# Kernel optimization log

Measured on AMD Instinct MI355X. Metric: run time of the kernel, lower is better.

The kernel has to match this reference:

```python
import jax, jax.numpy as jnp
import numpy as np
from jax import lax

MAX_W = 4           # max_subword_block_width
DOWNSAMPLE = 2      # downsample_rate


def setup_inputs() -> dict:
    key = jax.random.key(0)
    k1, k2, k3, k4 = jax.random.split(key, 4)
    B, E, L, K = 8, 512, 4096, 5
    x = jax.random.normal(k1, (B, E, L), dtype=jnp.float32)
    conv_w = jax.random.normal(k2, (E, E, K), dtype=jnp.float32) * (1.0 / np.sqrt(E * K))
    conv_b = jax.random.normal(k3, (E,), dtype=jnp.float32) * 0.02
    score_w = jax.random.normal(k4, (E,), dtype=jnp.float32) * (1.0 / np.sqrt(E))
    return {"x": x, "conv_w": conv_w, "conv_b": conv_b, "score_w": score_w}


def reference(x, conv_w, conv_b, score_w):
    B, E, L = x.shape  # `length` captured BEFORE conv, as in the torch code
    # pre-GBST conv, VALID padding: length becomes L - K + 1
    y = lax.conv_general_dilated(
        x, conv_w, window_strides=(1,), padding='VALID',
        dimension_numbers=('NCH', 'OIH', 'NCH')) + conv_b[None, :, None]
    L2 = y.shape[-1]
    seqs, scores = [], []
    for w in range(1, MAX_W + 1):
        pad = (-L2) % w
        yp = jnp.pad(y, ((0, 0), (0, 0), (0, pad)))  # zero-pad to multiple of w
        nb = yp.shape[-1] // w
        pooled = yp.reshape(B, E, nb, w).mean(-1)          # avg_pool1d(kernel=w, stride=w)
        sc = jnp.einsum('ben,e->bn', pooled, score_w)      # Linear(E,1,bias=False)
        rs = jnp.repeat(pooled, w, axis=-1)                # repeat_interleave
        rsc = jnp.repeat(sc, w, axis=-1)
        cur = rs.shape[-1]
        if cur < L:  # re-pad with zeros up to the ORIGINAL (pre-conv) length
            rs = jnp.pad(rs, ((0, 0), (0, 0), (0, L - cur)))
            rsc = jnp.pad(rsc, ((0, 0), (0, L - cur)))
        seqs.append(rs[:, :, :L])
        scores.append(rsc[:, :L])
    S = jnp.stack(seqs, axis=-1)                           # [B,E,L,W]
    A = jax.nn.softmax(jnp.stack(scores, axis=-1), axis=-1)  # [B,L,W]
    out = jnp.einsum('belw,blw->bel', S, A)                # softmax-weighted combine
    r = DOWNSAMPLE
    Ld = (L // r) * r
    out = out[:, :, :Ld].reshape(B, E, L // r, r).mean(-1)  # final avg_pool1d
    return out
```

## Files before the change

### kernel.cpp

```cpp
#include <hip/hip_runtime.h>
#include <stdint.h>

#define E_DIM 512
#define L_IN  4096
#define L_OUT 4092
#define KW    5
#define B_DIM 8
#define L2P   4096
#define L_DS  2048
#define LP    4160

typedef __attribute__((ext_vector_type(8))) short short8;
typedef __attribute__((ext_vector_type(4))) float f32x4;

__device__ __forceinline__ unsigned short f2bf(float f) {
    uint32_t u = __float_as_uint(f);
    u += 0x7fffu + ((u >> 16) & 1);
    return (unsigned short)(u >> 16);
}
__device__ __forceinline__ float bf2f(unsigned short h) {
    return __uint_as_float((uint32_t)h << 16);
}

__global__ __launch_bounds__(256)
void xt_kernel(const float* __restrict__ x, unsigned short* __restrict__ Xt)
{
    const int b  = blockIdx.z;
    const int i0 = blockIdx.y * 64;
    const int l0 = blockIdx.x * 64;
    __shared__ float T[64][65];
    const int tid = threadIdx.x;

    const int ir = tid >> 4;
    const int cq = (tid & 15) * 4;
    #pragma unroll
    for (int jj = 0; jj < 4; ++jj) {
        int i = jj * 16 + ir;
        float4 v = make_float4(0.f, 0.f, 0.f, 0.f);
        if (l0 < L_IN)
            v = *reinterpret_cast<const float4*>(
                &x[((size_t)b * E_DIM + i0 + i) * L_IN + l0 + cq]);
        T[i][cq + 0] = v.x; T[i][cq + 1] = v.y;
        T[i][cq + 2] = v.z; T[i][cq + 3] = v.w;
    }
    __syncthreads();
    const int h  = tid & 31;
    const int rq = tid >> 5;
    #pragma unroll
    for (int j = 0; j < 8; ++j) {
        int lr = j * 8 + rq;
        ushort2 o;
        o.x = f2bf(T[2 * h][lr]);
        o.y = f2bf(T[2 * h + 1][lr]);
        *reinterpret_cast<ushort2*>(
            &Xt[((size_t)b * LP + l0 + lr) * E_DIM + i0 + 2 * h]) = o;
    }
}

__global__ __launch_bounds__(256)
void wt_kernel(const float* __restrict__ w, unsigned short* __restrict__ Wt)
{
    int idx = blockIdx.x * 256 + threadIdx.x;
    if (idx >= E_DIM * E_DIM) return;
    #pragma unroll
    for (int k = 0; k < KW; ++k)
        Wt[(size_t)k * E_DIM * E_DIM + idx] = f2bf(w[(size_t)idx * KW + k]);
}

#define XB_BYTES 17408
#define N_XCH    (XB_BYTES / 1024)
#define WOFF     (2 * XB_BYTES)
#define WS_BYTES (5 * 128 * 64)
#define N_WCH    (WS_BYTES / 1024)
#define LDS_BYTES (WOFF + WS_BYTES)

__global__ __launch_bounds__(256, 2)
void conv_mfma(const unsigned short* __restrict__ Xt,
               const unsigned short* __restrict__ Wt,
               const float* __restrict__ bias,
               const float* __restrict__ sw,
               unsigned short* __restrict__ y,
               float* __restrict__ sp)
{
    __shared__ __align__(16) unsigned char lds[LDS_BYTES];
    const int l0 = blockIdx.x * 256;
    const int e0 = blockIdx.y * 128;
    const int b  = blockIdx.z;
    const int tid  = threadIdx.x;
    const int lane = tid & 63;
    const int wv   = tid >> 6;
    const int wr = wv >> 1, wc = wv & 1;
    const int lr = lane & 15, lg = lane >> 4;
    const int ln4r = lane >> 2;
    const int xswz = ((lane & 3) ^ ((lane >> 3) & 3)) * 8;

    const int aBase = WOFF + (wr * 64 + lr) * 64
                    + ((lg ^ ((lr >> 1) & 3)) << 4);
    int bBase[KW];
    #pragma unroll
    for (int kt = 0; kt < KW; ++kt)
        bBase[kt] = (wc * 128 + lr + kt) * 64
                  + ((lg ^ (((lr + kt) >> 1) & 3)) << 4);

    const unsigned short* xt_base =
        Xt + ((size_t)b * LP + l0) * E_DIM + xswz;

    auto stageX = [&](int buf, int i0) {
        for (int cch = wv; cch < N_XCH; cch += 4) {
            int row = cch * 16 + ln4r;
            const unsigned short* gp = xt_base + (size_t)row * E_DIM + i0;
            __builtin_amdgcn_global_load_lds(
                (const __attribute__((address_space(1))) void*)gp,
                (__attribute__((address_space(3))) void*)(lds + buf * XB_BYTES + cch * 1024),
                16, 0, 0);
        }
    };
    auto stageW = [&](int i0) {
        for (int cch = wv; cch < N_WCH; cch += 4) {
            int rk = cch * 16 + ln4r;
            int k = rk >> 7, er = rk & 127;
            const unsigned short* gp =
                Wt + ((size_t)k * E_DIM + e0 + er) * E_DIM + i0 + xswz;
            __builtin_amdgcn_global_load_lds(
                (const __attribute__((address_space(1))) void*)gp,
                (__attribute__((address_space(3))) void*)(lds + WOFF + cch * 1024),
                16, 0, 0);
        }
    };

    f32x4 acc[4][8] = {};

    stageX(0, 0);
    stageW(0);
    asm volatile("s_waitcnt vmcnt(0)" ::: "memory");
    __builtin_amdgcn_s_barrier();

    for (int ks = 0; ks < 16; ++ks) {
        const int par = ks & 1;
        if (ks < 15) stageX(par ^ 1, (ks + 1) * 32);

        #pragma unroll
        for (int kt = 0; kt < KW; ++kt) {
            short8 aF[4], bF[8];
            #pragma unroll
            for (int m = 0; m < 4; ++m)
                aF[m] = *reinterpret_cast<const short8*>(
                    &lds[aBase + (kt * 128 + m * 16) * 64]);
            #pragma unroll
            for (int n = 0; n < 8; ++n)
                bF[n] = *reinterpret_cast<const short8*>(
                    &lds[par * XB_BYTES + bBase[kt] + n * 1024]);
            #pragma unroll
            for (int m = 0; m < 4; ++m)
                #pragma unroll
                for (int n = 0; n < 8; ++n)
                    acc[m][n] = __builtin_amdgcn_mfma_f32_16x16x32_bf16(
                        aF[m], bF[n], acc[m][n], 0, 0, 0);
        }

        if (ks < 15) {
            __builtin_amdgcn_s_barrier();
            stageW((ks + 1) * 32);
            asm volatile("s_waitcnt vmcnt(0)" ::: "memory");
            __builtin_amdgcn_s_barrier();
        }
    }

    float spn[8] = {};
    #pragma unroll
    for (int m = 0; m < 4; ++m)
        #pragma unroll
        for (int q = 0; q < 4; ++q) {
            int e = e0 + wr * 64 + m * 16 + lg * 4 + q;
            float bv = bias[e];
            float wv_s = sw[e];
            unsigned short* yr =
                y + ((size_t)b * E_DIM + e) * L2P + l0 + wc * 128 + lr;
            #pragma unroll
            for (int n = 0; n < 8; ++n) {
                float v = acc[m][n][q] + bv;
                yr[n * 16] = f2bf(v);
                spn[n] = fmaf(v, wv_s, spn[n]);
            }
        }
    #pragma unroll
    for (int n = 0; n < 8; ++n) {
        float p = spn[n];
        p += __shfl_xor(p, 16);
        p += __shfl_xor(p, 32);
        if (lane < 16) {
            int l = l0 + wc * 128 + n * 16 + lane;
            sp[((size_t)b * L2P + l) * 8 + blockIdx.y * 2 + wr] = p;
        }
    }
}

__global__ __launch_bounds__(256)
void weight_kernel(const float* __restrict__ sp, float* __restrict__ A)
{
    const int b  = blockIdx.y;
    const int l0 = blockIdx.x * 256;
    const int tid = threadIdx.x;
    __shared__ float sl[260];

    for (int idx = tid; idx < 260; idx += 256) {
        int l = l0 - 2 + idx;
        float v = 0.f;
        if (l >= 0 && l < L_OUT) {
            const float* p = &sp[((size_t)b * L2P + l) * 8];
            v = ((p[0] + p[1]) + (p[2] + p[3])) + ((p[4] + p[5]) + (p[6] + p[7]));
        }
        sl[idx] = v;
    }
    __syncthreads();

    const int l = l0 + tid;
    if (l >= L_OUT) return;
    #define SL(i) sl[(i) - (l0 - 2)]
    float sc0 = SL(l);
    int n2 = l & ~1;
    float sc1 = 0.5f * (SL(n2) + SL(n2 + 1));
    int n3 = (l / 3) * 3;
    float sc2 = (1.f / 3.f) * (SL(n3) + SL(n3 + 1) + SL(n3 + 2));
    int n4 = l & ~3;
    float sc3 = 0.25f * (SL(n4) + SL(n4 + 1) + SL(n4 + 2) + SL(n4 + 3));
    #undef SL

    float m  = fmaxf(fmaxf(sc0, sc1), fmaxf(sc2, sc3));
    float e0 = __expf(sc0 - m), e1 = __expf(sc1 - m);
    float e2 = __expf(sc2 - m), e3 = __expf(sc3 - m);
    float inv = 1.f / (e0 + e1 + e2 + e3);

    float4 av = make_float4(e0 * inv, e1 * inv, e2 * inv, e3 * inv);
    *reinterpret_cast<float4*>(&A[((size_t)b * L2P + l) * 4]) = av;
}

typedef __attribute__((ext_vector_type(8))) unsigned short u16x8;

__global__ __launch_bounds__(256)
void combine_kernel(const unsigned short* __restrict__ y,
                    const float* __restrict__ A, float* __restrict__ out)
{
    const int e = blockIdx.x;
    const int b = blockIdx.y;
    const int tid = threadIdx.x;
    __shared__ float ys[L2P];

    const unsigned short* yrow = y + ((size_t)b * E_DIM + e) * L2P;
    #pragma unroll
    for (int j = 0; j < 2; ++j) {
        int base = (tid + j * 256) * 8;
        u16x8 v = *reinterpret_cast<const u16x8*>(&yrow[base]);
        #pragma unroll
        for (int t = 0; t < 8; ++t) ys[base + t] = bf2f(v[t]);
    }
    __syncthreads();

    const float* Ab = A + (size_t)b * L2P * 4;
    float* orow = out + ((size_t)b * E_DIM + e) * L_DS;
    #pragma unroll
    for (int j = 0; j < 8; ++j) {
        int m = tid + j * 256;
        float acc = 0.f;
        #pragma unroll
        for (int r = 0; r < 2; ++r) {
            int l = 2 * m + r;
            if (l < L_OUT) {
                const float4 a4 = *reinterpret_cast<const float4*>(&Ab[l * 4]);
                float t = a4.x * ys[l];
                int n2 = l & ~1;
                t += a4.y * 0.5f * (ys[n2] + ys[n2 + 1]);
                int n3 = (l / 3) * 3;
                t += a4.z * (1.f / 3.f) * (ys[n3] + ys[n3 + 1] + ys[n3 + 2]);
                int n4 = l & ~3;
                t += a4.w * 0.25f * (ys[n4] + ys[n4 + 1] + ys[n4 + 2] + ys[n4 + 3]);
                acc += t;
            }
        }
        orow[m] = 0.5f * acc;
    }
}

extern "C" void kernel_launch(void* const* d_in, const int* in_sizes, int n_in,
                              void* d_out, int out_size, void* d_ws, size_t ws_size,
                              hipStream_t stream)
{
    const float* x  = (const float*)d_in[0];
    const float* w  = (const float*)d_in[1];
    const float* bb = (const float*)d_in[2];
    const float* sw = (const float*)d_in[3];
    float* out = (float*)d_out;

    unsigned short* Y = (unsigned short*)d_ws;
    float* SP = (float*)(Y + (size_t)B_DIM * E_DIM * L2P);
    float* A  = SP + (size_t)B_DIM * L2P * 8;
    unsigned short* Xt = (unsigned short*)(A + (size_t)B_DIM * L2P * 4);
    unsigned short* Wt = Xt + (size_t)B_DIM * LP * E_DIM;

    xt_kernel<<<dim3(LP / 64, E_DIM / 64, B_DIM), 256, 0, stream>>>(x, Xt);
    wt_kernel<<<dim3(E_DIM * E_DIM / 256), 256, 0, stream>>>(w, Wt);
    conv_mfma<<<dim3(L2P / 256, E_DIM / 128, B_DIM), 256, 0, stream>>>(Xt, Wt, bb, sw, Y, SP);
    weight_kernel<<<dim3(L2P / 256, B_DIM), 256, 0, stream>>>(SP, A);
    combine_kernel<<<dim3(E_DIM, B_DIM), 256, 0, stream>>>(Y, A, out);
}
```

Measured before the change: 119.7 us.

## Pipeline weight taps through a three-slot LDS ring with per-tap barriers

The full 5-tap weight slab, which used to be loaded with an exposed vmcnt(0) wait after each K-step, is replaced by a 3-slot ring of per-tap weight slices. Each slice is prefetched two taps ahead and overlaps with the MFMA work, using partial vmcnt waits. This shrinks LDS use, which may allow more residency, and hides the weight-load latency. In exchange there are two barriers per tap instead of per K-step, plus s_setprio around the MFMA bursts.

Measured after the change: 116.1 us. 3.0% less time.

```diff
diff --git a/kernel.cpp b/kernel.cpp
--- a/kernel.cpp
+++ b/kernel.cpp
@@ -21,6 +21,11 @@
 __device__ __forceinline__ float bf2f(unsigned short h) {
     return __uint_as_float((uint32_t)h << 16);
 }
+__device__ __forceinline__ int mod3(int v) {
+    if (v >= 6) v -= 6;
+    if (v >= 3) v -= 3;
+    return v;
+}
 
 __global__ __launch_bounds__(256)
 void xt_kernel(const float* __restrict__ x, unsigned short* __restrict__ Xt)
@@ -67,12 +72,10 @@
         Wt[(size_t)k * E_DIM * E_DIM + idx] = f2bf(w[(size_t)idx * KW + k]);
 }
 
-#define XB_BYTES 17408
-#define N_XCH    (XB_BYTES / 1024)
-#define WOFF     (2 * XB_BYTES)
-#define WS_BYTES (5 * 128 * 64)
-#define N_WCH    (WS_BYTES / 1024)
-#define LDS_BYTES (WOFF + WS_BYTES)
+#define XB_BYTES  17408
+#define WOFF      (2 * XB_BYTES)
+#define WSL_BYTES 8192
+#define LDS_BYTES (WOFF + 3 * WSL_BYTES)
 
 __global__ __launch_bounds__(256, 2)
 void conv_mfma(const unsigned short* __restrict__ Xt,
@@ -94,8 +97,7 @@
     const int ln4r = lane >> 2;
     const int xswz = ((lane & 3) ^ ((lane >> 3) & 3)) * 8;
 
-    const int aBase = WOFF + (wr * 64 + lr) * 64
-                    + ((lg ^ ((lr >> 1) & 3)) << 4);
+    const int aOff = (wr * 64 + lr) * 64 + ((lg ^ ((lr >> 1) & 3)) << 4);
     int bBase[KW];
     #pragma unroll
     for (int kt = 0; kt < KW; ++kt)
@@ -106,7 +108,7 @@
         Xt + ((size_t)b * LP + l0) * E_DIM + xswz;
 
     auto stageX = [&](int buf, int i0) {
-        for (int cch = wv; cch < N_XCH; cch += 4) {
+        for (int cch = wv; cch < 17; cch += 4) {
             int row = cch * 16 + ln4r;
             const unsigned short* gp = xt_base + (size_t)row * E_DIM + i0;
             __builtin_amdgcn_global_load_lds(
@@ -115,15 +117,14 @@
                 16, 0, 0);
         }
     };
-    auto stageW = [&](int i0) {
-        for (int cch = wv; cch < N_WCH; cch += 4) {
-            int rk = cch * 16 + ln4r;
-            int k = rk >> 7, er = rk & 127;
+    auto stageW = [&](int dstOff, int tap, int i0) {
+        for (int cch = wv; cch < 8; cch += 4) {
+            int er = cch * 16 + ln4r;
             const unsigned short* gp =
-                Wt + ((size_t)k * E_DIM + e0 + er) * E_DIM + i0 + xswz;
+                Wt + ((size_t)tap * E_DIM + e0 + er) * E_DIM + i0 + xswz;
             __builtin_amdgcn_global_load_lds(
                 (const __attribute__((address_space(1))) void*)gp,
-                (__attribute__((address_space(3))) void*)(lds + WOFF + cch * 1024),
+                (__attribute__((address_space(3))) void*)(lds + dstOff + cch * 1024),
                 16, 0, 0);
         }
     };
@@ -131,39 +132,50 @@
     f32x4 acc[4][8] = {};
 
     stageX(0, 0);
-    stageW(0);
+    stageW(WOFF + 0 * WSL_BYTES, 0, 0);
+    stageW(WOFF + 1 * WSL_BYTES, 1, 0);
     asm volatile("s_waitcnt vmcnt(0)" ::: "memory");
     __builtin_amdgcn_s_barrier();
 
+    int s0 = 0;
     for (int ks = 0; ks < 16; ++ks) {
-        const int par = ks & 1;
-        if (ks < 15) stageX(par ^ 1, (ks + 1) * 32);
-
+        const int par  = ks & 1;
+        const int xoff = par * XB_BYTES;
         #pragma unroll
         for (int kt = 0; kt < KW; ++kt) {
+            const int wsl = WOFF + mod3(s0 + kt) * WSL_BYTES;
             short8 aF[4], bF[8];
             #pragma unroll
             for (int m = 0; m < 4; ++m)
                 aF[m] = *reinterpret_cast<const short8*>(
-                    &lds[aBase + (kt * 128 + m * 16) * 64]);
+                    &lds[wsl + aOff + m * 1024]);
             #pragma unroll
             for (int n = 0; n < 8; ++n)
                 bF[n] = *reinterpret_cast<const short8*>(
-                    &lds[par * XB_BYTES + bBase[kt] + n * 1024]);
+                    &lds[xoff + bBase[kt] + n * 1024]);
+
+            if (kt == 0 && ks < 15) stageX(par ^ 1, (ks + 1) * 32);
+            if (!(ks == 15 && kt >= 3)) {
+                const int dst = WOFF + mod3(s0 + kt + 2) * WSL_BYTES;
+                if (kt <= 2) stageW(dst, kt + 2, ks * 32);
+                else         stageW(dst, kt - 3, (ks + 1) * 32);
+            }
+
+            if (kt == 0) asm volatile("s_waitcnt vmcnt(6)" ::: "memory");
+            else         asm volatile("s_waitcnt vmcnt(2)" ::: "memory");
+            __builtin_amdgcn_s_barrier();
+
+            __builtin_amdgcn_s_setprio(1);
             #pragma unroll
             for (int m = 0; m < 4; ++m)
                 #pragma unroll
                 for (int n = 0; n < 8; ++n)
                     acc[m][n] = __builtin_amdgcn_mfma_f32_16x16x32_bf16(
                         aF[m], bF[n], acc[m][n], 0, 0, 0);
-        }
-
-        if (ks < 15) {
+            __builtin_amdgcn_s_setprio(0);
             __builtin_amdgcn_s_barrier();
-            stageW((ks + 1) * 32);
-            asm volatile("s_waitcnt vmcnt(0)" ::: "memory");
-            __builtin_amdgcn_s_barrier();
-        }
+        }
+        s0 += 2; if (s0 >= 3) s0 -= 3;
     }
 
     float spn[8] = {};
```

## Load conv weights directly into registers in MFMA fragment layout, drop LDS staging

Applied to the files above, without the earlier changes.

Weights are pre-permuted into a fragment-ordered layout so each wave loads its A operands straight from global memory into registers with one coalesced 16-byte load per lane. A register double buffer prefetches the next kt/ks weights during the MFMAs. This removes the LDS weight staging and one of the two barriers per K-step, which also cuts LDS use and may improve occupancy. In exchange, each wave issues its own global weight loads, relying on L2 hits and latency hiding by the prefetch.

Measured after the change: 122.5 us. +2.4%, slower.

```diff
diff --git a/kernel.cpp b/kernel.cpp
--- a/kernel.cpp
+++ b/kernel.cpp
@@ -12,6 +12,7 @@
 
 typedef __attribute__((ext_vector_type(8))) short short8;
 typedef __attribute__((ext_vector_type(4))) float f32x4;
+typedef __attribute__((ext_vector_type(8))) unsigned short u16x8;
 
 __device__ __forceinline__ unsigned short f2bf(float f) {
     uint32_t u = __float_as_uint(f);
@@ -58,25 +59,33 @@
 }
 
 __global__ __launch_bounds__(256)
-void wt_kernel(const float* __restrict__ w, unsigned short* __restrict__ Wt)
-{
-    int idx = blockIdx.x * 256 + threadIdx.x;
-    if (idx >= E_DIM * E_DIM) return;
-    #pragma unroll
-    for (int k = 0; k < KW; ++k)
-        Wt[(size_t)k * E_DIM * E_DIM + idx] = f2bf(w[(size_t)idx * KW + k]);
-}
-
-#define XB_BYTES 17408
-#define N_XCH    (XB_BYTES / 1024)
-#define WOFF     (2 * XB_BYTES)
-#define WS_BYTES (5 * 128 * 64)
-#define N_WCH    (WS_BYTES / 1024)
-#define LDS_BYTES (WOFF + WS_BYTES)
+void wt2_kernel(const float* __restrict__ w, unsigned short* __restrict__ Wt2)
+{
+    const int idx  = blockIdx.x * 256 + threadIdx.x;
+    const int lane = idx & 63;
+    const int seg  = idx >> 6;
+    const int ks = seg & 15;
+    const int kt = (seg >> 4) % KW;
+    const int em = seg / (KW * 16);
+    const int e  = (em >> 2) * 64 + (em & 3) * 16 + (lane & 15);
+    const int i0 = ks * 32 + (lane >> 4) * 8;
+
+    unsigned short o[8];
+    #pragma unroll
+    for (int j = 0; j < 8; ++j)
+        o[j] = f2bf(w[((size_t)e * E_DIM + i0 + j) * KW + kt]);
+    *reinterpret_cast<u16x8*>(&Wt2[(size_t)seg * 512 + lane * 8]) =
+        *reinterpret_cast<u16x8*>(o);
+}
+
+#define XS_ROWS  272
+#define XS_BYTES (XS_ROWS * 64)
+#define N_XCH    (XS_BYTES / 1024)
+#define LDS_BYTES (2 * XS_BYTES)
 
 __global__ __launch_bounds__(256, 2)
 void conv_mfma(const unsigned short* __restrict__ Xt,
-               const unsigned short* __restrict__ Wt,
+               const unsigned short* __restrict__ Wt2,
                const float* __restrict__ bias,
                const float* __restrict__ sw,
                unsigned short* __restrict__ y,
@@ -94,16 +103,17 @@
     const int ln4r = lane >> 2;
     const int xswz = ((lane & 3) ^ ((lane >> 3) & 3)) * 8;
 
-    const int aBase = WOFF + (wr * 64 + lr) * 64
-                    + ((lg ^ ((lr >> 1) & 3)) << 4);
-    int bBase[KW];
-    #pragma unroll
-    for (int kt = 0; kt < KW; ++kt)
-        bBase[kt] = (wc * 128 + lr + kt) * 64
-                  + ((lg ^ (((lr + kt) >> 1) & 3)) << 4);
-
     const unsigned short* xt_base =
         Xt + ((size_t)b * LP + l0) * E_DIM + xswz;
+    const unsigned short* wt_base =
+        Wt2 + (size_t)(blockIdx.y * 2 + wr) * 4 * (KW * 16) * 512 + lane * 8;
+
+    int bAddr[KW];
+    #pragma unroll
+    for (int kt = 0; kt < KW; ++kt) {
+        const int rB = wc * 128 + lr + kt;
+        bAddr[kt] = rB * 64 + ((lg ^ ((rB >> 1) & 3)) << 4);
+    }
 
     auto stageX = [&](int buf, int i0) {
         for (int cch = wv; cch < N_XCH; cch += 4) {
@@ -111,56 +121,59 @@
             const unsigned short* gp = xt_base + (size_t)row * E_DIM + i0;
             __builtin_amdgcn_global_load_lds(
                 (const __attribute__((address_space(1))) void*)gp,
-                (__attribute__((address_space(3))) void*)(lds + buf * XB_BYTES + cch * 1024),
+                (__attribute__((address_space(3))) void*)
+                    (lds + buf * XS_BYTES + cch * 1024),
                 16, 0, 0);
         }
     };
-    auto stageW = [&](int i0) {
-        for (int cch = wv; cch < N_WCH; cch += 4) {
-            int rk = cch * 16 + ln4r;
-            int k = rk >> 7, er = rk & 127;
-            const unsigned short* gp =
-                Wt + ((size_t)k * E_DIM + e0 + er) * E_DIM + i0 + xswz;
-            __builtin_amdgcn_global_load_lds(
-                (const __attribute__((address_space(1))) void*)gp,
-                (__attribute__((address_space(3))) void*)(lds + WOFF + cch * 1024),
-                16, 0, 0);
-        }
-    };
 
     f32x4 acc[4][8] = {};
+    short8 aC[4], aN[4];
 
     stageX(0, 0);
-    stageW(0);
+    #pragma unroll
+    for (int m = 0; m < 4; ++m)
+        aC[m] = *reinterpret_cast<const short8*>(
+            wt_base + (size_t)(m * (KW * 16)) * 512);
     asm volatile("s_waitcnt vmcnt(0)" ::: "memory");
     __builtin_amdgcn_s_barrier();
 
     for (int ks = 0; ks < 16; ++ks) {
-        const int par = ks & 1;
+        const int par  = ks & 1;
+        const int xoff = par * XS_BYTES;
         if (ks < 15) stageX(par ^ 1, (ks + 1) * 32);
 
         #pragma unroll
         for (int kt = 0; kt < KW; ++kt) {
-            short8 aF[4], bF[8];
-            #pragma unroll
-            for (int m = 0; m < 4; ++m)
-                aF[m] = *reinterpret_cast<const short8*>(
-                    &lds[aBase + (kt * 128 + m * 16) * 64]);
+            if (kt < KW - 1) {
+                #pragma unroll
+                for (int m = 0; m < 4; ++m)
+                    aN[m] = *reinterpret_cast<const short8*>(
+                        wt_base + (size_t)(m * (KW * 16) + (kt + 1) * 16 + ks) * 512);
+            } else if (ks < 15) {
+                #pragma unroll
+                for (int m = 0; m < 4; ++m)
+                    aN[m] = *reinterpret_cast<const short8*>(
+                        wt_base + (size_t)(m * (KW * 16) + (ks + 1)) * 512);
+            }
+            short8 bF[8];
             #pragma unroll
             for (int n = 0; n < 8; ++n)
                 bF[n] = *reinterpret_cast<const short8*>(
-                    &lds[par * XB_BYTES + bBase[kt] + n * 1024]);
+                    &lds[xoff + bAddr[kt] + n * 1024]);
             #pragma unroll
             for (int m = 0; m < 4; ++m)
                 #pragma unroll
                 for (int n = 0; n < 8; ++n)
                     acc[m][n] = __builtin_amdgcn_mfma_f32_16x16x32_bf16(
-                        aF[m], bF[n], acc[m][n], 0, 0, 0);
+                        aC[m], bF[n], acc[m][n], 0, 0, 0);
+            if (kt < KW - 1 || ks < 15) {
+                #pragma unroll
+                for (int m = 0; m < 4; ++m) aC[m] = aN[m];
+            }
         }
 
         if (ks < 15) {
-            __builtin_amdgcn_s_barrier();
-            stageW((ks + 1) * 32);
             asm volatile("s_waitcnt vmcnt(0)" ::: "memory");
             __builtin_amdgcn_s_barrier();
         }
@@ -234,8 +247,6 @@
     float4 av = make_float4(e0 * inv, e1 * inv, e2 * inv, e3 * inv);
     *reinterpret_cast<float4*>(&A[((size_t)b * L2P + l) * 4]) = av;
 }
-
-typedef __attribute__((ext_vector_type(8))) unsigned short u16x8;
 
 __global__ __launch_bounds__(256)
 void combine_kernel(const unsigned short* __restrict__ y,
@@ -294,12 +305,12 @@
     unsigned short* Y = (unsigned short*)d_ws;
     float* SP = (float*)(Y + (size_t)B_DIM * E_DIM * L2P);
     float* A  = SP + (size_t)B_DIM * L2P * 8;
-    unsigned short* Xt = (unsigned short*)(A + (size_t)B_DIM * L2P * 4);
-    unsigned short* Wt = Xt + (size_t)B_DIM * LP * E_DIM;
+    unsigned short* Xt  = (unsigned short*)(A + (size_t)B_DIM * L2P * 4);
+    unsigned short* Wt2 = Xt + (size_t)B_DIM * LP * E_DIM;
 
     xt_kernel<<<dim3(LP / 64, E_DIM / 64, B_DIM), 256, 0, stream>>>(x, Xt);
-    wt_kernel<<<dim3(E_DIM * E_DIM / 256), 256, 0, stream>>>(w, Wt);
-    conv_mfma<<<dim3(L2P / 256, E_DIM / 128, B_DIM), 256, 0, stream>>>(Xt, Wt, bb, sw, Y, SP);
+    wt2_kernel<<<dim3(640), 256, 0, stream>>>(w, Wt2);
+    conv_mfma<<<dim3(L2P / 256, E_DIM / 128, B_DIM), 256, 0, stream>>>(Xt, Wt2, bb, sw, Y, SP);
     weight_kernel<<<dim3(L2P / 256, B_DIM), 256, 0, stream>>>(SP, A);
     combine_kernel<<<dim3(E_DIM, B_DIM), 256, 0, stream>>>(Y, A, out);
 }
```
